# Performance work log

Measured on AMD Instinct MI355X. Metric: run time of the kernel, lower is better.

## Reference

```python
import jax, jax.numpy as jnp
import numpy as np

# --- static config (matches init_kwargs) ---
N = 10000          # nodes
E = 160000         # edges
MULT = 16          # multiplicity (in and out)
NL = 2             # number of irreps (lvals = [0, 1])
DIM = 4            # 1 + 3 spherical dims
EDGE_DIM = 32
HID = 128
RANK = 8           # low-rank radial weight rank
H = 4              # attention heads
HM = MULT // H     # head multiplicity
IDX = np.array([0, 1, 1, 1])  # irrep index for each of the DIM positions


def _radial(ef, w1, bb1, wl, bl, wr, br):
    """Low-rank radial weight: (E, edge_dim) -> (E, NL*MULT, NL*MULT)."""
    h = jax.nn.gelu(ef @ w1 + bb1, approximate=False)
    left = (h @ wl + bl).reshape(-1, NL * MULT, RANK)
    right = (h @ wr + br).reshape(-1, RANK, NL * MULT)
    return left @ right


def _conv(b1, b2, ef, f, src, w1, bb1, wl, bl, wr, br):
    """Equivariant convolution: gather -> basis contract -> radial bmm -> basis."""
    rw = _radial(ef, w1, bb1, wl, bl, wr, br)          # (E, 2*MULT, 2*MULT)
    f_src = f[src]                                      # (E, MULT, DIM)
    t = jnp.einsum('emd,edl->eml', f_src, b1)           # (E, MULT, NL)
    t = t.reshape(E, MULT * NL)                         # row-major, matches torch view
    t = jnp.einsum('erc,ec->er', rw, t)                 # (E, NL*MULT)
    t = t.reshape(E, MULT, NL)                          # (E, out_mult, nl2)
    return jnp.einsum('eml,eld->emd', t, b2)            # (E, MULT, DIM)


def reference(b1, b2, edge_feats, f, src_idx, dst_idx,
              q_w, q_b,
              k_w1, k_b1, k_wl, k_bl, k_wr, k_br,
              v_w1, v_b1, v_wl, v_bl, v_wr, v_br):
    # --- Q: equivariant linear on node features (per-irrep weights) ---
    W = q_w.reshape(NL, MULT, MULT)[IDX]                # (DIM, out_mult, in_mult)
    q = jnp.einsum('dom,nmd->nod', W, f)                # (N, MULT, DIM)
    q = q.at[:, :, 0].add(q_b[:, 0])                    # bias on scalar (l=0) slot

    # --- K, V: equivariant convolutions over edges ---
    k = _conv(b1, b2, edge_feats, f, src_idx, k_w1, k_b1, k_wl, k_bl, k_wr, k_br)
    v = _conv(b1, b2, edge_feats, f, src_idx, v_w1, v_b1, v_wl, v_bl, v_wr, v_br)

    # --- multi-head node_wise attention scores ---
    qh = q.reshape(N, H, HM * DIM)
    kh = k.reshape(E, H, HM * DIM)
    scale = jnp.sqrt(jnp.asarray(HM * DIM, q.dtype))
    scores = jnp.sum(qh[dst_idx] * kh, axis=-1) / scale  # (E, H)

    # --- segment softmax over edges grouped by destination node ---
    m = jax.ops.segment_max(scores, dst_idx, num_segments=N)       # (N, H)
    ex = jnp.exp(scores - m[dst_idx])
    den = jax.ops.segment_sum(ex, dst_idx, num_segments=N)         # (N, H)
    alpha = ex / jnp.maximum(den[dst_idx], 1e-9)                   # (E, H)

    # --- weighted scatter-reduce of values ---
    vh = v.reshape(E, H, HM * DIM)
    out = jax.ops.segment_sum(alpha[..., None] * vh, dst_idx, num_segments=N)
    return out.reshape(N, MULT, DIM)


def setup_inputs() -> dict:
    key = jax.random.key(0)
    ks = jax.random.split(key, 24)
    s = 0.05
    inp = {
        'b1': jax.random.normal(ks[0], (E, DIM, NL), jnp.float32),
        'b2': jax.random.normal(ks[1], (E, NL, DIM), jnp.float32),
        'edge_feats': jax.random.normal(ks[2], (E, EDGE_DIM), jnp.float32),
        'f': jax.random.normal(ks[3], (N, MULT, DIM), jnp.float32),
        'src_idx': jax.random.randint(ks[4], (E,), 0, N),
        'dst_idx': jax.random.randint(ks[5], (E,), 0, N),
        # Q equivariant linear
        'q_w': jax.random.normal(ks[6], (NL * MULT, MULT), jnp.float32) * s,
        'q_b': jnp.zeros((MULT, 1), jnp.float32),
    }
    for i, p in enumerate(['k', 'v']):
        base = 8 + i * 6
        inp[p + '_w1'] = jax.random.normal(ks[base + 0], (EDGE_DIM, HID), jnp.float32) * s
        inp[p + '_b1'] = jnp.zeros((HID,), jnp.float32)
        inp[p + '_wl'] = jax.random.normal(ks[base + 2], (HID, NL * MULT * RANK), jnp.float32) * s
        inp[p + '_bl'] = jnp.zeros((NL * MULT * RANK,), jnp.float32)
        inp[p + '_wr'] = jax.random.normal(ks[base + 4], (HID, RANK * NL * MULT), jnp.float32) * s
        inp[p + '_br'] = jnp.zeros((RANK * NL * MULT,), jnp.float32)
    return inp
```

## Files before the change

### kernel.cpp

```cpp
#include <hip/hip_runtime.h>
#include <hip/hip_bf16.h>
#include <math.h>

#define NNODES 10000
#define NEDGE  160000

typedef unsigned short u16;
using bf16x8 = __attribute__((ext_vector_type(8))) short;
using u16x8  = __attribute__((ext_vector_type(8))) unsigned short;
using f32x4  = __attribute__((ext_vector_type(4))) float;

static __device__ __forceinline__ u16 f2bf(float x) {
  unsigned u = __float_as_uint(x);
  u += 0x7FFFu + ((u >> 16) & 1u);
  return (u16)(u >> 16);
}
static __device__ __forceinline__ float bf2f(u16 h) {
  return __uint_as_float(((unsigned)h) << 16);
}
static __device__ __forceinline__ unsigned pack_bf16(float a, float b) {
  __hip_bfloat162 h = __float22bfloat162_rn(make_float2(a, b));
  return *(unsigned*)&h;
}
static __device__ __forceinline__ float fast_gelu(float x) {
  float y = x * __builtin_fmaf(0.07135481283f, x * x, 1.5957691216f);
  float e = __expf(y);
  return x - x * __builtin_amdgcn_rcpf(e + 1.0f);
}

__global__ void zero_cnt_kernel(int* __restrict__ cnt) {
  int i = blockIdx.x * 256 + threadIdx.x;
  if (i < NNODES) cnt[i] = 0;
}

__global__ void __launch_bounds__(256) setup_kernel(
    const float* __restrict__ kwr, const float* __restrict__ kwl,
    const float* __restrict__ vwr, const float* __restrict__ vwl,
    u16* __restrict__ Wsw,
    const float* __restrict__ kw1, const float* __restrict__ vw1,
    u16* __restrict__ W1sw,
    const float* __restrict__ f, const float* __restrict__ qw,
    const float* __restrict__ qb, float* __restrict__ q,
    const int* __restrict__ dst, int* __restrict__ cnt) {
  int b = blockIdx.x, tid = threadIdx.x;
  if (b < 512) {
    int idx = b * 256 + tid;
    int slot = idx >> 15;
    int w = idx & 32767;
    int j = w & 7, lane = (w >> 3) & 63, ks = (w >> 9) & 3, tg = w >> 11;
    int k   = ks * 32 + ((lane >> 4) << 3) + j;
    int col = (tg << 4) + (lane & 15);
    const float* s = (slot == 0) ? kwr : (slot == 1) ? kwl : (slot == 2) ? vwr : vwl;
    Wsw[idx] = f2bf(s[k * 256 + col]);
  } else if (b < 544) {
    int idx = (b - 512) * 256 + tid;
    int slot = idx >> 12;
    int w = idx & 4095;
    int j = w & 7, lane = (w >> 3) & 63, nt = w >> 9;
    int k   = ((lane >> 4) << 3) + j;
    int col = (nt << 4) + (lane & 15);
    const float* s = (slot == 0) ? kw1 : vw1;
    W1sw[idx] = f2bf(s[k * 128 + col]);
  } else if (b < 1169) {
    int i = (b - 544) * 256 + tid;
    if (i >= NNODES * 16) return;
    int n = i >> 4, o = i & 15;
    const float* frow = f + (size_t)n * 64;
    float o0 = 0.f, o1 = 0.f, o2 = 0.f, o3 = 0.f;
#pragma unroll
    for (int m = 0; m < 16; ++m) {
      float w0 = qw[o * 16 + m];
      float w1 = qw[(16 + o) * 16 + m];
      o0 += w0 * frow[m * 4 + 0];
      o1 += w1 * frow[m * 4 + 1];
      o2 += w1 * frow[m * 4 + 2];
      o3 += w1 * frow[m * 4 + 3];
    }
    o0 += qb[o];
    float4 r = make_float4(o0, o1, o2, o3);
    *(float4*)(q + (size_t)i * 4) = r;
  } else {
    int e = (b - 1169) * 256 + tid;
    atomicAdd(&cnt[dst[e]], 1);
  }
}

__global__ void __launch_bounds__(1024) csr_scan_kernel(
    const int* __restrict__ cnt, int* __restrict__ rowptr, int* __restrict__ cursor) {
  __shared__ int part[1024];
  int t = threadIdx.x;
  int base = t * 10;
  int s = 0;
#pragma unroll
  for (int i = 0; i < 10; ++i) { int idx = base + i; if (idx < NNODES) s += cnt[idx]; }
  part[t] = s;
  __syncthreads();
  for (int o = 1; o < 1024; o <<= 1) {
    int v = (t >= o) ? part[t - o] : 0;
    __syncthreads();
    part[t] += v;
    __syncthreads();
  }
  int run = (t == 0) ? 0 : part[t - 1];
#pragma unroll
  for (int i = 0; i < 10; ++i) {
    int idx = base + i;
    if (idx < NNODES) { rowptr[idx] = run; cursor[idx] = run; run += cnt[idx]; }
  }
  if (t == 1023) rowptr[NNODES] = run;
}

__global__ void __launch_bounds__(256) fill_t_kernel(
    const int* __restrict__ dst, const int* __restrict__ src,
    const float* __restrict__ f, const float* __restrict__ b1,
    const float* __restrict__ b2, const float* __restrict__ ef,
    int* __restrict__ cursor, char* __restrict__ comb) {
  int e = blockIdx.x * 256 + threadIdx.x;
  int n = dst[e];
  int pos = atomicAdd(&cursor[n], 1);
  char* rb = comb + (size_t)pos * 192;
  const float* frow = f + (size_t)src[e] * 64;
  const float* be = b1 + (size_t)e * 8;
  float b[8];
#pragma unroll
  for (int k = 0; k < 8; ++k) b[k] = be[k];
  uint4* tp = (uint4*)rb;
#pragma unroll
  for (int mh = 0; mh < 4; ++mh) {
    unsigned pk[4];
#pragma unroll
    for (int mi = 0; mi < 4; ++mi) {
      int m = mh * 4 + mi;
      float f0 = frow[m * 4 + 0], f1 = frow[m * 4 + 1], f2 = frow[m * 4 + 2], f3 = frow[m * 4 + 3];
      float t0 = f0 * b[0] + f1 * b[2] + f2 * b[4] + f3 * b[6];
      float t1 = f0 * b[1] + f1 * b[3] + f2 * b[5] + f3 * b[7];
      pk[mi] = pack_bf16(t0, t1);
    }
    tp[mh] = make_uint4(pk[0], pk[1], pk[2], pk[3]);
  }
  const float* efe = ef + (size_t)e * 32;
#pragma unroll
  for (int g = 0; g < 4; ++g) {
    float4 v0 = *(const float4*)&efe[g * 8];
    float4 v1 = *(const float4*)&efe[g * 8 + 4];
    tp[4 + g] = make_uint4(pack_bf16(v0.x, v0.y), pack_bf16(v0.z, v0.w),
                           pack_bf16(v1.x, v1.y), pack_bf16(v1.z, v1.w));
  }
  const float* b2e = b2 + (size_t)e * 8;
  *(float4*)(rb + 128) = *(const float4*)&b2e[0];
  *(float4*)(rb + 144) = *(const float4*)&b2e[4];
  *(int*)(rb + 160) = n;
}

__global__ void __launch_bounds__(512) conv_fused_kernel(
    const char* __restrict__ comb, const u16* __restrict__ w1sw,
    const float* __restrict__ b1h,
    const u16* __restrict__ wsw_r, const float* __restrict__ br,
    const u16* __restrict__ wsw_l, const float* __restrict__ bl,
    const float* __restrict__ qbuf, float* __restrict__ exs,
    u16* __restrict__ kv) {
  __shared__ alignas(16) u16 sA[64 * 136];
  __shared__ alignas(16) u16 t_s[64 * 40];
  __shared__ alignas(16) float b2_s[64 * 12];
  __shared__ alignas(16) float u_s[64 * 12];
  __shared__ alignas(16) float t2_pool[64 * 36];
  float* t2_s = t2_pool;
  u16*   efs  = (u16*)t2_pool;

  int tid = threadIdx.x;
  int wave = tid >> 6, lane = tid & 63, quad = lane >> 4, l16 = lane & 15;
  size_t i0 = (size_t)blockIdx.x * 64;

  if (tid < 256) {
    int row = tid >> 2, seg = tid & 3;
    *(uint4*)&efs[row * 40 + seg * 8] =
        *(const uint4*)(comb + (i0 + row) * 192 + 64 + seg * 16);
    if (tid < 128) {
      int r2 = tid >> 1, half = tid & 1;
      *(float4*)&b2_s[r2 * 12 + half * 4] =
          *(const float4*)(comb + (i0 + r2) * 192 + 128 + half * 16);
    }
  } else {
    int j = tid - 256;
    int row = j >> 2, seg = j & 3;
    *(uint4*)&t_s[row * 40 + seg * 8] =
        *(const uint4*)(comb + (i0 + row) * 192 + seg * 16);
  }
  __syncthreads();

  {
    bf16x8 aw = *(const bf16x8*)&w1sw[(size_t)(wave * 64 + lane) * 8];
    float4 bias_h = *(const float4*)&b1h[wave * 16 + quad * 4];
#pragma unroll
    for (int nt = 0; nt < 4; ++nt) {
      bf16x8 be = *(const bf16x8*)&efs[(nt * 16 + l16) * 40 + quad * 8];
      f32x4 acch = __builtin_amdgcn_mfma_f32_16x16x32_bf16(aw, be, (f32x4){0.f, 0.f, 0.f, 0.f}, 0, 0, 0);
      unsigned p0 = pack_bf16(fast_gelu(acch[0] + bias_h.x), fast_gelu(acch[1] + bias_h.y));
      unsigned p1 = pack_bf16(fast_gelu(acch[2] + bias_h.z), fast_gelu(acch[3] + bias_h.w));
      *(uint2*)&sA[(nt * 16 + l16) * 136 + wave * 16 + quad * 4] = make_uint2(p0, p1);
    }
  }
  __syncthreads();

  f32x4 accr[2][4], accl[2][4];
#pragma unroll
  for (int mtl = 0; mtl < 2; ++mtl)
#pragma unroll
    for (int nt = 0; nt < 4; ++nt) {
      accr[mtl][nt] = (f32x4){0.f, 0.f, 0.f, 0.f};
      accl[mtl][nt] = (f32x4){0.f, 0.f, 0.f, 0.f};
    }
#pragma unroll
  for (int ks = 0; ks < 4; ++ks) {
    bf16x8 bfrag[4];
#pragma unroll
    for (int nt = 0; nt < 4; ++nt)
      bfrag[nt] = *(const bf16x8*)&sA[(nt * 16 + l16) * 136 + ks * 32 + quad * 8];
#pragma unroll
    for (int mtl = 0; mtl < 2; ++mtl) {
      int mtg = wave * 2 + mtl;
      bf16x8 ar = *(const bf16x8*)&wsw_r[(size_t)((mtg * 4 + ks) * 64 + lane) * 8];
      bf16x8 al = *(const bf16x8*)&wsw_l[(size_t)((mtg * 4 + ks) * 64 + lane) * 8];
#pragma unroll
      for (int nt = 0; nt < 4; ++nt) {
        accr[mtl][nt] = __builtin_amdgcn_mfma_f32_16x16x32_bf16(ar, bfrag[nt], accr[mtl][nt], 0, 0, 0);
        accl[mtl][nt] = __builtin_amdgcn_mfma_f32_16x16x32_bf16(al, bfrag[nt], accl[mtl][nt], 0, 0, 0);
      }
    }
  }

  float4 brv[2], blv[2];
#pragma unroll
  for (int mtl = 0; mtl < 2; ++mtl) {
    int colb = (wave * 2 + mtl) * 16 + quad * 4;
    brv[mtl] = *(const float4*)&br[colb];
    blv[mtl] = *(const float4*)&bl[colb];
  }

#pragma unroll
  for (int nt = 0; nt < 4; ++nt) {
    int e = nt * 16 + l16;
    ushort4 ta = *(const ushort4*)&t_s[e * 40 + 4 * quad];
    ushort4 tb = *(const ushort4*)&t_s[e * 40 + 16 + 4 * quad];
    float s = (accr[0][nt][0] + brv[0].x) * bf2f(ta.x)
            + (accr[0][nt][1] + brv[0].y) * bf2f(ta.y)
            + (accr[0][nt][2] + brv[0].z) * bf2f(ta.z)
            + (accr[0][nt][3] + brv[0].w) * bf2f(ta.w)
            + (accr[1][nt][0] + brv[1].x) * bf2f(tb.x)
            + (accr[1][nt][1] + brv[1].y) * bf2f(tb.y)
            + (accr[1][nt][2] + brv[1].z) * bf2f(tb.z)
            + (accr[1][nt][3] + brv[1].w) * bf2f(tb.w);
    s += __shfl_xor(s, 16);
    s += __shfl_xor(s, 32);
    if (quad == 0) u_s[e * 12 + wave] = s;
  }
  __syncthreads();

#pragma unroll
  for (int nt = 0; nt < 4; ++nt) {
    int e = nt * 16 + l16;
    float4 uv = *(const float4*)&u_s[e * 12 + 4 * (quad & 1)];
#pragma unroll
    for (int mtl = 0; mtl < 2; ++mtl) {
      float s = (accl[mtl][nt][0] + blv[mtl].x) * uv.x
              + (accl[mtl][nt][1] + blv[mtl].y) * uv.y
              + (accl[mtl][nt][2] + blv[mtl].z) * uv.z
              + (accl[mtl][nt][3] + blv[mtl].w) * uv.w;
      s += __shfl_xor(s, 16);
      if ((quad & 1) == 0)
        t2_s[e * 36 + 4 * wave + 2 * mtl + (quad >> 1)] = s;
    }
  }
  __syncthreads();

  {
    int e = tid >> 3, j = tid & 7;
    float4 t2 = *(const float4*)&t2_s[e * 36 + 4 * j];
    float4 b2a = *(const float4*)&b2_s[e * 12 + 0];
    float4 b2b = *(const float4*)&b2_s[e * 12 + 4];
    float v0 = t2.x * b2a.x + t2.y * b2b.x;
    float v1 = t2.x * b2a.y + t2.y * b2b.y;
    float v2 = t2.x * b2a.z + t2.y * b2b.z;
    float v3 = t2.x * b2a.w + t2.y * b2b.w;
    float v4 = t2.z * b2a.x + t2.w * b2b.x;
    float v5 = t2.z * b2a.y + t2.w * b2b.y;
    float v6 = t2.z * b2a.z + t2.w * b2b.z;
    float v7 = t2.z * b2a.w + t2.w * b2b.w;
    if (exs) {
      int n = *(const int*)(comb + (i0 + e) * 192 + 160);
      const float* qr = qbuf + (size_t)n * 64 + j * 8;
      float4 qa = *(const float4*)&qr[0];
      float4 qc = *(const float4*)&qr[4];
      float s = v0 * qa.x + v1 * qa.y + v2 * qa.z + v3 * qa.w
              + v4 * qc.x + v5 * qc.y + v6 * qc.z + v7 * qc.w;
      s += __shfl_xor(s, 1);
      if ((j & 1) == 0)
        exs[(i0 + e) * 4 + (j >> 1)] = __expf(s * 0.25f);
    } else {
      unsigned q0 = pack_bf16(v0, v1);
      unsigned q1 = pack_bf16(v2, v3);
      unsigned q2 = pack_bf16(v4, v5);
      unsigned q3 = pack_bf16(v6, v7);
      *(uint4*)&kv[(i0 + e) * 64 + j * 8] = make_uint4(q0, q1, q2, q3);
    }
  }
}

__global__ void __launch_bounds__(256) attn_gather_kernel(
    const float* __restrict__ exs, const u16* __restrict__ kvv,
    const int* __restrict__ rowptr, float* __restrict__ outp) {
  int tid = threadIdx.x;
  int node = blockIdx.x * 4 + (tid >> 6);
  int lane = tid & 63, h = lane >> 4;
  int beg = rowptr[node], end = rowptr[node + 1];
  float num = 0.f, den = 0.f;
  int idx = beg;
  for (; idx + 2 <= end; idx += 2) {
    float e0 = exs[(size_t)idx * 4 + h];
    float e1 = exs[(size_t)(idx + 1) * 4 + h];
    float v0 = bf2f(kvv[(size_t)idx * 64 + lane]);
    float v1 = bf2f(kvv[(size_t)(idx + 1) * 64 + lane]);
    num += e0 * v0 + e1 * v1;
    den += e0 + e1;
  }
  if (idx < end) {
    float e0 = exs[(size_t)idx * 4 + h];
    num += e0 * bf2f(kvv[(size_t)idx * 64 + lane]);
    den += e0;
  }
  outp[(size_t)node * 64 + lane] = num / fmaxf(den, 1e-9f);
}

extern "C" void kernel_launch(void* const* d_in, const int* in_sizes, int n_in,
                              void* d_out, int out_size, void* d_ws, size_t ws_size,
                              hipStream_t stream) {
  const float* b1  = (const float*)d_in[0];
  const float* b2  = (const float*)d_in[1];
  const float* ef  = (const float*)d_in[2];
  const float* f   = (const float*)d_in[3];
  const int*   src = (const int*)d_in[4];
  const int*   dst = (const int*)d_in[5];
  const float* qw  = (const float*)d_in[6];
  const float* qb  = (const float*)d_in[7];
  const float* kw1 = (const float*)d_in[8];
  const float* kb1 = (const float*)d_in[9];
  const float* kwl = (const float*)d_in[10];
  const float* kbl = (const float*)d_in[11];
  const float* kwr = (const float*)d_in[12];
  const float* kbr = (const float*)d_in[13];
  const float* vw1 = (const float*)d_in[14];
  const float* vb1 = (const float*)d_in[15];
  const float* vwl = (const float*)d_in[16];
  const float* vbl = (const float*)d_in[17];
  const float* vwr = (const float*)d_in[18];
  const float* vbr = (const float*)d_in[19];
  float* outp = (float*)d_out;

  char* ws = (char*)d_ws;
  size_t off = 0;
  auto alloc = [&](size_t bytes) {
    char* p = ws + off;
    off += (bytes + 511) & ~(size_t)511;
    return p;
  };
  u16*   Wsw  = (u16*)  alloc((size_t)4 * 32768 * 2);
  u16*   W1sw = (u16*)  alloc((size_t)2 * 4096 * 2);
  char*  comb = (char*) alloc((size_t)NEDGE * 192);
  u16*   kvv  = (u16*)  alloc((size_t)NEDGE * 64 * 2);
  float* exb  = (float*)alloc((size_t)NEDGE * 4 * 4);
  float* qbuf = (float*)alloc((size_t)NNODES * 64 * 4);
  int*   cnt    = (int*)alloc((size_t)NNODES * 4);
  int*   rowptr = (int*)alloc((size_t)(NNODES + 1) * 4);
  int*   cursor = (int*)alloc((size_t)NNODES * 4);

  zero_cnt_kernel<<<40, 256, 0, stream>>>(cnt);
  setup_kernel<<<1794, 256, 0, stream>>>(kwr, kwl, vwr, vwl, Wsw,
                                         kw1, vw1, W1sw,
                                         f, qw, qb, qbuf, dst, cnt);
  csr_scan_kernel<<<1, 1024, 0, stream>>>(cnt, rowptr, cursor);
  fill_t_kernel<<<625, 256, 0, stream>>>(dst, src, f, b1, b2, ef,
                                         cursor, comb);

  conv_fused_kernel<<<2500, 512, 0, stream>>>(comb, W1sw + 0 * 4096, kb1,
                                              Wsw + 0 * 32768, kbr,
                                              Wsw + 1 * 32768, kbl,
                                              qbuf, exb, nullptr);
  conv_fused_kernel<<<2500, 512, 0, stream>>>(comb, W1sw + 1 * 4096, vb1,
                                              Wsw + 2 * 32768, vbr,
                                              Wsw + 3 * 32768, vbl,
                                              qbuf, nullptr, kvv);

  attn_gather_kernel<<<2500, 256, 0, stream>>>(exb, kvv, rowptr, outp);
}
```

Before: 246.2 us.

## Build CSR in one shared-memory kernel and merge K/V conv launches

Replaces the zero/global-atomic count/scan sequence with a single-block kernel that builds the destination histogram with shared-memory atomics and scans it, removing two launches and the global atomic pass. The two conv_fused launches are merged into one grid of twice the size, with even blocks computing K attention scores and odd blocks computing V, so neighbouring blocks share the same edge tile in cache and one launch is saved. The single-block histogram over all edges serialises that work on one CU, and the merged conv adds per-block pointer selection.

```diff
diff --git a/kernel.cpp b/kernel.cpp
--- a/kernel.cpp
+++ b/kernel.cpp
@@ -28,9 +28,46 @@
   return x - x * __builtin_amdgcn_rcpf(e + 1.0f);
 }
 
-__global__ void zero_cnt_kernel(int* __restrict__ cnt) {
-  int i = blockIdx.x * 256 + threadIdx.x;
-  if (i < NNODES) cnt[i] = 0;
+__global__ void __launch_bounds__(1024) csr_build_kernel(
+    const int* __restrict__ dst, int* __restrict__ rowptr, int* __restrict__ cursor) {
+  __shared__ int hist[NNODES];
+  __shared__ int part[1024];
+  int t = threadIdx.x;
+  for (int i = t; i < NNODES; i += 1024) hist[i] = 0;
+  __syncthreads();
+  const int4* d4 = (const int4*)dst;
+  for (int i = t; i < NEDGE / 4; i += 1024) {
+    int4 v = d4[i];
+    atomicAdd(&hist[v.x], 1);
+    atomicAdd(&hist[v.y], 1);
+    atomicAdd(&hist[v.z], 1);
+    atomicAdd(&hist[v.w], 1);
+  }
+  __syncthreads();
+  int base = t * 10;
+  int local[10];
+  int s = 0;
+#pragma unroll
+  for (int i = 0; i < 10; ++i) {
+    int idx = base + i;
+    local[i] = (idx < NNODES) ? hist[idx] : 0;
+    s += local[i];
+  }
+  part[t] = s;
+  __syncthreads();
+  for (int o = 1; o < 1024; o <<= 1) {
+    int v = (t >= o) ? part[t - o] : 0;
+    __syncthreads();
+    part[t] += v;
+    __syncthreads();
+  }
+  int run = (t == 0) ? 0 : part[t - 1];
+#pragma unroll
+  for (int i = 0; i < 10; ++i) {
+    int idx = base + i;
+    if (idx < NNODES) { rowptr[idx] = run; cursor[idx] = run; run += local[i]; }
+  }
+  if (t == 1023) rowptr[NNODES] = run;
 }
 
 __global__ void __launch_bounds__(256) setup_kernel(
@@ -40,8 +77,7 @@
     const float* __restrict__ kw1, const float* __restrict__ vw1,
     u16* __restrict__ W1sw,
     const float* __restrict__ f, const float* __restrict__ qw,
-    const float* __restrict__ qb, float* __restrict__ q,
-    const int* __restrict__ dst, int* __restrict__ cnt) {
+    const float* __restrict__ qb, float* __restrict__ q) {
   int b = blockIdx.x, tid = threadIdx.x;
   if (b < 512) {
     int idx = b * 256 + tid;
@@ -61,7 +97,7 @@
     int col = (nt << 4) + (lane & 15);
     const float* s = (slot == 0) ? kw1 : vw1;
     W1sw[idx] = f2bf(s[k * 128 + col]);
-  } else if (b < 1169) {
+  } else {
     int i = (b - 544) * 256 + tid;
     if (i >= NNODES * 16) return;
     int n = i >> 4, o = i & 15;
@@ -79,35 +115,7 @@
     o0 += qb[o];
     float4 r = make_float4(o0, o1, o2, o3);
     *(float4*)(q + (size_t)i * 4) = r;
-  } else {
-    int e = (b - 1169) * 256 + tid;
-    atomicAdd(&cnt[dst[e]], 1);
-  }
-}
-
-__global__ void __launch_bounds__(1024) csr_scan_kernel(
-    const int* __restrict__ cnt, int* __restrict__ rowptr, int* __restrict__ cursor) {
-  __shared__ int part[1024];
-  int t = threadIdx.x;
-  int base = t * 10;
-  int s = 0;
-#pragma unroll
-  for (int i = 0; i < 10; ++i) { int idx = base + i; if (idx < NNODES) s += cnt[idx]; }
-  part[t] = s;
-  __syncthreads();
-  for (int o = 1; o < 1024; o <<= 1) {
-    int v = (t >= o) ? part[t - o] : 0;
-    __syncthreads();
-    part[t] += v;
-    __syncthreads();
-  }
-  int run = (t == 0) ? 0 : part[t - 1];
-#pragma unroll
-  for (int i = 0; i < 10; ++i) {
-    int idx = base + i;
-    if (idx < NNODES) { rowptr[idx] = run; cursor[idx] = run; run += cnt[idx]; }
-  }
-  if (t == 1023) rowptr[NNODES] = run;
+  }
 }
 
 __global__ void __launch_bounds__(256) fill_t_kernel(
@@ -153,10 +161,13 @@
 }
 
 __global__ void __launch_bounds__(512) conv_fused_kernel(
-    const char* __restrict__ comb, const u16* __restrict__ w1sw,
-    const float* __restrict__ b1h,
-    const u16* __restrict__ wsw_r, const float* __restrict__ br,
-    const u16* __restrict__ wsw_l, const float* __restrict__ bl,
+    const char* __restrict__ comb,
+    const u16* __restrict__ w1sw_k, const float* __restrict__ b1h_k,
+    const u16* __restrict__ wswr_k, const float* __restrict__ br_k,
+    const u16* __restrict__ wswl_k, const float* __restrict__ bl_k,
+    const u16* __restrict__ w1sw_v, const float* __restrict__ b1h_v,
+    const u16* __restrict__ wswr_v, const float* __restrict__ br_v,
+    const u16* __restrict__ wswl_v, const float* __restrict__ bl_v,
     const float* __restrict__ qbuf, float* __restrict__ exs,
     u16* __restrict__ kv) {
   __shared__ alignas(16) u16 sA[64 * 136];
@@ -169,7 +180,15 @@
 
   int tid = threadIdx.x;
   int wave = tid >> 6, lane = tid & 63, quad = lane >> 4, l16 = lane & 15;
-  size_t i0 = (size_t)blockIdx.x * 64;
+  bool kmode = (blockIdx.x & 1) == 0;
+  size_t i0 = (size_t)(blockIdx.x >> 1) * 64;
+
+  const u16*   w1sw = kmode ? w1sw_k : w1sw_v;
+  const float* b1h  = kmode ? b1h_k  : b1h_v;
+  const u16*   wsw_r = kmode ? wswr_k : wswr_v;
+  const float* br    = kmode ? br_k   : br_v;
+  const u16*   wsw_l = kmode ? wswl_k : wswl_v;
+  const float* bl    = kmode ? bl_k   : bl_v;
 
   if (tid < 256) {
     int row = tid >> 2, seg = tid & 3;
@@ -286,7 +305,7 @@
     float v5 = t2.z * b2a.y + t2.w * b2b.y;
     float v6 = t2.z * b2a.z + t2.w * b2b.z;
     float v7 = t2.z * b2a.w + t2.w * b2b.w;
-    if (exs) {
+    if (kmode) {
       int n = *(const int*)(comb + (i0 + e) * 192 + 160);
       const float* qr = qbuf + (size_t)n * 64 + j * 8;
       float4 qa = *(const float4*)&qr[0];
@@ -369,26 +388,24 @@
   u16*   kvv  = (u16*)  alloc((size_t)NEDGE * 64 * 2);
   float* exb  = (float*)alloc((size_t)NEDGE * 4 * 4);
   float* qbuf = (float*)alloc((size_t)NNODES * 64 * 4);
-  int*   cnt    = (int*)alloc((size_t)NNODES * 4);
   int*   rowptr = (int*)alloc((size_t)(NNODES + 1) * 4);
   int*   cursor = (int*)alloc((size_t)NNODES * 4);
 
-  zero_cnt_kernel<<<40, 256, 0, stream>>>(cnt);
-  setup_kernel<<<1794, 256, 0, stream>>>(kwr, kwl, vwr, vwl, Wsw,
+  csr_build_kernel<<<1, 1024, 0, stream>>>(dst, rowptr, cursor);
+  setup_kernel<<<1169, 256, 0, stream>>>(kwr, kwl, vwr, vwl, Wsw,
                                          kw1, vw1, W1sw,
-                                         f, qw, qb, qbuf, dst, cnt);
-  csr_scan_kernel<<<1, 1024, 0, stream>>>(cnt, rowptr, cursor);
+                                         f, qw, qb, qbuf);
   fill_t_kernel<<<625, 256, 0, stream>>>(dst, src, f, b1, b2, ef,
                                          cursor, comb);
 
-  conv_fused_kernel<<<2500, 512, 0, stream>>>(comb, W1sw + 0 * 4096, kb1,
+  conv_fused_kernel<<<5000, 512, 0, stream>>>(comb,
+                                              W1sw + 0 * 4096, kb1,
                                               Wsw + 0 * 32768, kbr,
                                               Wsw + 1 * 32768, kbl,
-                                              qbuf, exb, nullptr);
-  conv_fused_kernel<<<2500, 512, 0, stream>>>(comb, W1sw + 1 * 4096, vb1,
+                                              W1sw + 1 * 4096, vb1,
                                               Wsw + 2 * 32768, vbr,
                                               Wsw + 3 * 32768, vbl,
-                                              qbuf, nullptr, kvv);
+                                              qbuf, exb, kvv);
 
   attn_gather_kernel<<<2500, 256, 0, stream>>>(exb, kvv, rowptr, outp);
 }
```

Measured after the change: 245.8 us. No clear change (-0.1%).
